# Kernel optimization log

Hardware: AMD Instinct MI355X
Metric: run time of the kernel (lower is better)

## Reference

```python
import jax, jax.numpy as jnp
import numpy as np

PYR = 40000
N_PV, N_OLM, N_BIST = 2100, 1800, 1200
N_SEPT = 100
DT = 1.0
E_EXC, E_INH = 3.0, -0.5


def _sparse_uniform(key, n_out, n_in, conn, w_max, no_autapse=False):
    km, kw = jax.random.split(key)
    mask = jax.random.uniform(km, (n_out, n_in)) < conn
    w = jnp.where(mask, jax.random.uniform(kw, (n_out, n_in)) * w_max, 0.0)
    if no_autapse:
        w = w * (1.0 - jnp.eye(n_out))
    return w.astype(jnp.float32)


def setup_inputs() -> dict:
    key = jax.random.key(0)
    ks = jax.random.split(key, 24)
    inp = {}
    inp['pyr_spikes'] = jax.random.randint(ks[0], (PYR,), 0, 2, dtype=jnp.int32)
    inp['septal_gaba'] = jax.random.uniform(ks[1], (N_SEPT,), dtype=jnp.float32)
    inp['external_exc'] = jax.random.uniform(ks[2], (N_PV,), dtype=jnp.float32)
    inp['prev_pv_spikes'] = (jax.random.uniform(ks[3], (N_PV,)) < 0.1).astype(jnp.float32)
    inp['prev_olm_spikes'] = (jax.random.uniform(ks[4], (N_OLM,)) < 0.1).astype(jnp.float32)
    inp['prev_pv_v_mem'] = jax.random.uniform(ks[5], (N_PV,), dtype=jnp.float32)
    inp['pv_v'] = jax.random.uniform(ks[6], (N_PV,), dtype=jnp.float32)
    inp['olm_v'] = jax.random.uniform(ks[7], (N_OLM,), dtype=jnp.float32)
    inp['bist_v'] = jax.random.uniform(ks[8], (N_BIST,), dtype=jnp.float32)
    inp['pv_adapt'] = jnp.zeros((N_PV,), jnp.float32)
    inp['olm_adapt'] = jnp.zeros((N_OLM,), jnp.float32)
    inp['bist_adapt'] = jnp.zeros((N_BIST,), jnp.float32)
    # weights per WeightInitializer.sparse_uniform calls in __init__ (ca1_inhibitory branch)
    inp['pyr_to_pv'] = _sparse_uniform(ks[9], N_PV, PYR, 0.5, 0.0012)
    inp['pyr_to_olm'] = _sparse_uniform(ks[10], N_OLM, PYR, 0.3, 0.0006)
    inp['pyr_to_bist'] = _sparse_uniform(ks[11], N_BIST, PYR, 0.35, 0.0007)
    inp['pv_to_pyr'] = _sparse_uniform(ks[12], PYR, N_PV, 0.5, 0.003)
    inp['pv_to_pyr_gaba_b'] = _sparse_uniform(ks[13], PYR, N_PV, 0.5, 0.003 * 0.15)
    inp['olm_to_pyr'] = _sparse_uniform(ks[14], PYR, N_OLM, 0.5, 0.001)
    inp['bist_to_pyr'] = _sparse_uniform(ks[15], PYR, N_BIST, 0.55, 0.002)
    inp['pv_to_pv'] = _sparse_uniform(ks[16], N_PV, N_PV, 0.3, 0.0005, no_autapse=True)
    inp['olm_to_pv'] = _sparse_uniform(ks[17], N_PV, N_OLM, 0.2, 0.0004)
    gj = _sparse_uniform(ks[18], N_PV, N_PV, 0.5, 0.0003, no_autapse=True)
    inp['pv_gap'] = (gj + gj.T) * 0.5  # symmetrized gap junctions
    inp['septal_to_olm'] = (jnp.abs(jax.random.normal(ks[19], (N_OLM, N_SEPT))) * 0.5).astype(jnp.float32)
    return inp


def _split_exc(g, nmda_ratio=0.3):
    g = jnp.maximum(g, 0.0)  # conductances are nonnegative
    return g * (1.0 - nmda_ratio), g * nmda_ratio


def _lif_step(v, adapt, g_ampa, g_nmda, g_gaba_a, tau_mem, v_th, v_reset, tau_adapt, adapt_inc):
    # conductance-based LIF: leak toward 0 (v_rest), synaptic currents toward reversals
    i_syn = (g_ampa + g_nmda) * (E_EXC - v) + g_gaba_a * (E_INH - v)
    v_new = v + (DT / tau_mem) * (-v + i_syn)
    spk = (v_new >= (v_th + adapt)).astype(v.dtype)
    v_out = jnp.where(spk > 0, v_reset, v_new)
    adapt_new = adapt * (1.0 - DT / tau_adapt) + adapt_inc * spk
    return spk, v_out, adapt_new


def reference(pyr_spikes, septal_gaba, external_exc, prev_pv_spikes, prev_olm_spikes,
              prev_pv_v_mem, pv_v, olm_v, bist_v, pv_adapt, olm_adapt, bist_adapt,
              pyr_to_pv, pyr_to_olm, pyr_to_bist, pv_to_pyr, pv_to_pyr_gaba_b,
              olm_to_pyr, bist_to_pyr, pv_to_pv, olm_to_pv, pv_gap, septal_to_olm):
    pyr_f = pyr_spikes.astype(jnp.float32)
    pv_exc = pyr_to_pv @ pyr_f
    olm_exc = pyr_to_olm @ pyr_f
    bist_exc = pyr_to_bist @ pyr_f
    pv_exc_from_pyr = pv_exc
    ext_mean = external_exc.mean()
    pv_exc = pv_exc + ext_mean * 0.3
    olm_exc = olm_exc + ext_mean * 0.1
    bist_exc = bist_exc + ext_mean * 0.2
    olm_g_inh = septal_to_olm @ septal_gaba
    pv_lateral = pv_to_pv @ prev_pv_spikes
    olm_to_pv_inhib = olm_to_pv @ prev_olm_spikes
    pv_exc = pv_exc - pv_lateral * 0.5 - olm_to_pv_inhib * 0.3
    # gap junctions: gated by mean pyramidal drive (traced condition -> where)
    drive = pv_exc_from_pyr.mean()
    gain = jnp.where(drive > 0.01, jnp.minimum(1.0, drive / 0.1), 0.0)
    pv_gap_current = pv_gap @ prev_pv_v_mem  # v @ W.T with symmetric-ish W
    pv_exc = pv_exc + pv_gap_current * 0.05 * gain
    pv_ga, pv_gn = _split_exc(pv_exc)
    olm_ga, olm_gn = _split_exc(olm_exc)
    bi_ga, bi_gn = _split_exc(bist_exc)
    zero_pv = jnp.zeros_like(pv_v)
    zero_bi = jnp.zeros_like(bist_v)
    pv_spk, _, _ = _lif_step(pv_v, pv_adapt, pv_ga, pv_gn, zero_pv, 7.0, 2.0, 0.0, 50.0, 0.05)
    olm_spk, _, _ = _lif_step(olm_v, olm_adapt, olm_ga, olm_gn, olm_g_inh, 25.0, 1.1, 0.0, 100.0, 0.2)
    bist_spk, _, _ = _lif_step(bist_v, bist_adapt, bi_ga, bi_gn, zero_bi, 12.0, 0.9, 0.0, 60.0, 0.08)
    perisomatic = pv_to_pyr @ pv_spk
    perisomatic_gaba_b = pv_to_pyr_gaba_b @ pv_spk
    olm_dendritic = olm_to_pyr @ olm_spk
    dendritic = olm_dendritic + bist_to_pyr @ bist_spk
    return (perisomatic, perisomatic_gaba_b, dendritic, olm_dendritic, pv_spk, olm_spk, bist_spk)
```

## Files before the change

### kernel.cpp

```cpp
#include <hip/hip_runtime.h>

#define PYR 40000
#define N_PV 2100
#define N_OLM 1800
#define N_BIST 1200
#define N_SEPT 100

#define WS_PV_RAW   0
#define WS_OLM_RAW  2100
#define WS_BIST_RAW 3900
#define WS_PV_LAT   5100
#define WS_OLM_IPV  7200
#define WS_GAP      9300
#define WS_OLM_GINH 11400

#define O_PERI 0
#define O_GABA 40000
#define O_DEND 80000
#define O_OLMD 120000
#define O_PVS  160000
#define O_OLMS 162100
#define O_BIS  163900

typedef float f4 __attribute__((ext_vector_type(4)));
typedef int   i4 __attribute__((ext_vector_type(4)));

__device__ __forceinline__ f4 ntload(const f4* p) { return __builtin_nontemporal_load(p); }

__device__ __forceinline__ float wave_reduce(float acc) {
    #pragma unroll
    for (int o = 32; o > 0; o >>= 1) acc += __shfl_down(acc, o, 64);
    return acc;
}

#define P1_BLOCKS (N_PV + N_OLM + N_BIST)
#define SMALL_BLOCKS ((3 * N_PV + N_OLM + 3) / 4)
__global__ __launch_bounds__(256) void k_big(
    const float* __restrict__ Wpv, const float* __restrict__ Wolm,
    const float* __restrict__ Wbi, const int* __restrict__ pyr,
    const float* __restrict__ Wpvpv, const float* __restrict__ Wolmpv,
    const float* __restrict__ Wgap,  const float* __restrict__ Wsept,
    const float* __restrict__ prev_pv, const float* __restrict__ prev_olm,
    const float* __restrict__ prev_vm, const float* __restrict__ sept_g,
    float* __restrict__ ws)
{
    int b = blockIdx.x;
    if (b < P1_BLOCKS) {
        const float* W; float* dst;
        if (b < N_PV)               { W = Wpv  + (size_t)b * PYR;                   dst = ws + WS_PV_RAW  + b; }
        else if (b < N_PV + N_OLM)  { int r = b - N_PV;         W = Wolm + (size_t)r * PYR; dst = ws + WS_OLM_RAW  + r; }
        else                        { int r = b - N_PV - N_OLM; W = Wbi  + (size_t)r * PYR; dst = ws + WS_BIST_RAW + r; }

        const f4* W4 = (const f4*)W;
        const i4* S4 = (const i4*)pyr;
        float acc = 0.0f;
        for (int j = threadIdx.x; j < PYR / 4; j += 256) {
            f4 w = ntload(W4 + j);
            i4 s = S4[j];
            acc += w.x * (float)s.x + w.y * (float)s.y + w.z * (float)s.z + w.w * (float)s.w;
        }
        acc = wave_reduce(acc);
        __shared__ float sm[4];
        int lane = threadIdx.x & 63, wv = threadIdx.x >> 6;
        if (lane == 0) sm[wv] = acc;
        __syncthreads();
        if (threadIdx.x == 0) *dst = sm[0] + sm[1] + sm[2] + sm[3];
        return;
    }
    int r = (b - P1_BLOCKS) * 4 + (threadIdx.x >> 6);
    int lane = threadIdx.x & 63;
    const float* W; const float* v; int len4; float* dst;
    if (r < N_PV)                   { W = Wpvpv  + (size_t)r * N_PV;               v = prev_pv;  len4 = N_PV / 4;   dst = ws + WS_PV_LAT  + r; }
    else if (r < 2 * N_PV)          { int i = r - N_PV;     W = Wolmpv + (size_t)i * N_OLM;  v = prev_olm; len4 = N_OLM / 4;  dst = ws + WS_OLM_IPV + i; }
    else if (r < 3 * N_PV)          { int i = r - 2 * N_PV; W = Wgap   + (size_t)i * N_PV;   v = prev_vm;  len4 = N_PV / 4;   dst = ws + WS_GAP     + i; }
    else if (r < 3 * N_PV + N_OLM)  { int i = r - 3 * N_PV; W = Wsept  + (size_t)i * N_SEPT; v = sept_g;   len4 = N_SEPT / 4; dst = ws + WS_OLM_GINH + i; }
    else return;

    const f4* W4 = (const f4*)W;
    const f4* V4 = (const f4*)v;
    float acc = 0.0f;
    for (int j = lane; j < len4; j += 64) {
        f4 w = ntload(W4 + j), x = V4[j];
        acc += w.x * x.x + w.y * x.y + w.z * x.z + w.w * x.w;
    }
    acc = wave_reduce(acc);
    if (lane == 0) *dst = acc;
}

__global__ __launch_bounds__(256) void k_lif(
    const float* __restrict__ ws, const float* __restrict__ ext,
    const float* __restrict__ pv_v,  const float* __restrict__ olm_v,  const float* __restrict__ bist_v,
    const float* __restrict__ pv_ad, const float* __restrict__ olm_ad, const float* __restrict__ bist_ad,
    float* __restrict__ out)
{
    __shared__ float s1[256], s2[256];
    float a = 0.0f, bsum = 0.0f;
    for (int i = threadIdx.x; i < N_PV; i += 256) { a += ext[i]; bsum += ws[WS_PV_RAW + i]; }
    s1[threadIdx.x] = a; s2[threadIdx.x] = bsum;
    __syncthreads();
    for (int o = 128; o > 0; o >>= 1) {
        if (threadIdx.x < o) { s1[threadIdx.x] += s1[threadIdx.x + o]; s2[threadIdx.x] += s2[threadIdx.x + o]; }
        __syncthreads();
    }
    float ext_mean = s1[0] / (float)N_PV;
    float drive    = s2[0] / (float)N_PV;
    float gain = (drive > 0.01f) ? fminf(1.0f, drive / 0.1f) : 0.0f;

    int t = blockIdx.x * 256 + threadIdx.x;
    if (t < N_PV) {
        float g = ws[WS_PV_RAW + t] + ext_mean * 0.3f
                - ws[WS_PV_LAT + t] * 0.5f - ws[WS_OLM_IPV + t] * 0.3f
                + ws[WS_GAP + t] * 0.05f * gain;
        g = fmaxf(g, 0.0f);
        float v = pv_v[t], ad = pv_ad[t];
        float isyn = g * (3.0f - v);
        float vn = v + (1.0f / 7.0f) * (-v + isyn);
        out[O_PVS + t] = (vn >= 2.0f + ad) ? 1.0f : 0.0f;
    } else if (t < N_PV + N_OLM) {
        int i = t - N_PV;
        float g = fmaxf(ws[WS_OLM_RAW + i] + ext_mean * 0.1f, 0.0f);
        float gi = ws[WS_OLM_GINH + i];
        float v = olm_v[i], ad = olm_ad[i];
        float isyn = g * (3.0f - v) + gi * (-0.5f - v);
        float vn = v + (1.0f / 25.0f) * (-v + isyn);
        out[O_OLMS + i] = (vn >= 1.1f + ad) ? 1.0f : 0.0f;
    } else if (t < N_PV + N_OLM + N_BIST) {
        int i = t - N_PV - N_OLM;
        float g = fmaxf(ws[WS_BIST_RAW + i] + ext_mean * 0.2f, 0.0f);
        float v = bist_v[i], ad = bist_ad[i];
        float isyn = g * (3.0f - v);
        float vn = v + (1.0f / 12.0f) * (-v + isyn);
        out[O_BIS + i] = (vn >= 0.9f + ad) ? 1.0f : 0.0f;
    }
}

__global__ __launch_bounds__(256) void k_phase2(
    const float* __restrict__ Wpp, const float* __restrict__ Wppb,
    const float* __restrict__ Wop, const float* __restrict__ Wbp,
    float* __restrict__ out)
{
    int r = blockIdx.x * 4 + (threadIdx.x >> 6);
    int lane = threadIdx.x & 63;
    int job = r / PYR;
    int p = r - job * PYR;

    if (job < 2) {
        const float* W = (job == 0 ? Wpp : Wppb) + (size_t)p * N_PV;
        const f4* W4 = (const f4*)W;
        const f4* V4 = (const f4*)(out + O_PVS);
        float acc = 0.0f;
        for (int j = lane; j < N_PV / 4; j += 64) {
            f4 w = ntload(W4 + j), x = V4[j];
            acc += w.x * x.x + w.y * x.y + w.z * x.z + w.w * x.w;
        }
        acc = wave_reduce(acc);
        if (lane == 0) out[(job == 0 ? O_PERI : O_GABA) + p] = acc;
    } else {
        const f4* Wo4 = (const f4*)(Wop + (size_t)p * N_OLM);
        const f4* Wb4 = (const f4*)(Wbp + (size_t)p * N_BIST);
        const f4* Vo4 = (const f4*)(out + O_OLMS);
        const f4* Vb4 = (const f4*)(out + O_BIS);
        float ao = 0.0f, ab = 0.0f;
        for (int j = lane; j < N_OLM / 4; j += 64) {
            f4 w = ntload(Wo4 + j), x = Vo4[j];
            ao += w.x * x.x + w.y * x.y + w.z * x.z + w.w * x.w;
        }
        for (int j = lane; j < N_BIST / 4; j += 64) {
            f4 w = ntload(Wb4 + j), x = Vb4[j];
            ab += w.x * x.x + w.y * x.y + w.z * x.z + w.w * x.w;
        }
        ao = wave_reduce(ao);
        ab = wave_reduce(ab);
        if (lane == 0) {
            out[O_OLMD + p] = ao;
            out[O_DEND + p] = ao + ab;
        }
    }
}

extern "C" void kernel_launch(void* const* d_in, const int* in_sizes, int n_in,
                              void* d_out, int out_size, void* d_ws, size_t ws_size,
                              hipStream_t stream)
{
    const int*   pyr     = (const int*)  d_in[0];
    const float* sept_g  = (const float*)d_in[1];
    const float* ext     = (const float*)d_in[2];
    const float* prev_pv = (const float*)d_in[3];
    const float* prev_olm= (const float*)d_in[4];
    const float* prev_vm = (const float*)d_in[5];
    const float* pv_v    = (const float*)d_in[6];
    const float* olm_v   = (const float*)d_in[7];
    const float* bist_v  = (const float*)d_in[8];
    const float* pv_ad   = (const float*)d_in[9];
    const float* olm_ad  = (const float*)d_in[10];
    const float* bist_ad = (const float*)d_in[11];
    const float* Wpyr_pv = (const float*)d_in[12];
    const float* Wpyr_olm= (const float*)d_in[13];
    const float* Wpyr_bi = (const float*)d_in[14];
    const float* Wpp     = (const float*)d_in[15];
    const float* Wppb    = (const float*)d_in[16];
    const float* Wop     = (const float*)d_in[17];
    const float* Wbp     = (const float*)d_in[18];
    const float* Wpvpv   = (const float*)d_in[19];
    const float* Wolmpv  = (const float*)d_in[20];
    const float* Wgap    = (const float*)d_in[21];
    const float* Wsept   = (const float*)d_in[22];

    float* ws  = (float*)d_ws;
    float* out = (float*)d_out;

    k_big<<<P1_BLOCKS + SMALL_BLOCKS, 256, 0, stream>>>(
        Wpyr_pv, Wpyr_olm, Wpyr_bi, pyr,
        Wpvpv, Wolmpv, Wgap, Wsept,
        prev_pv, prev_olm, prev_vm, sept_g, ws);
    k_lif<<<(N_PV + N_OLM + N_BIST + 255) / 256, 256, 0, stream>>>(
        ws, ext, pv_v, olm_v, bist_v, pv_ad, olm_ad, bist_ad, out);
    k_phase2<<<(3 * PYR) / 4, 256, 0, stream>>>(Wpp, Wppb, Wop, Wbp, out);
}
```

Measured before the change: 334.2 us.

## Fuse LIF step into first kernel via last-block atomic counter; unroll dot loops

The separate LIF kernel is removed. Its work now runs in the last block of the first kernel to finish, which detects itself with an atomic counter and thread fences, so one launch and its gap go away. Dot-product loops use compile-time trip counts with unrolling, which should give more loads in flight. This adds a memset launch, a serial LIF tail run by a single block, and atomic and fence overhead on every block.

```diff
diff --git a/kernel.cpp b/kernel.cpp
--- a/kernel.cpp
+++ b/kernel.cpp
@@ -13,6 +13,7 @@
 #define WS_OLM_IPV  7200
 #define WS_GAP      9300
 #define WS_OLM_GINH 11400
+#define WS_CNT      13200
 
 #define O_PERI 0
 #define O_GABA 40000
@@ -33,8 +34,31 @@
     return acc;
 }
 
+template<int LEN4>
+__device__ __forceinline__ float dot_row(const f4* __restrict__ W4,
+                                         const f4* __restrict__ V4, int lane) {
+    float acc = 0.0f;
+    constexpr int FULL = LEN4 / 64;
+    constexpr int TAIL = LEN4 % 64;
+    #pragma unroll
+    for (int it = 0; it < FULL; ++it) {
+        int j = lane + it * 64;
+        f4 w = ntload(W4 + j), x = V4[j];
+        acc += w.x * x.x + w.y * x.y + w.z * x.z + w.w * x.w;
+    }
+    if (TAIL && lane < TAIL) {
+        int j = FULL * 64 + lane;
+        f4 w = ntload(W4 + j), x = V4[j];
+        acc += w.x * x.x + w.y * x.y + w.z * x.z + w.w * x.w;
+    }
+    return acc;
+}
+
 #define P1_BLOCKS (N_PV + N_OLM + N_BIST)
-#define SMALL_BLOCKS ((3 * N_PV + N_OLM + 3) / 4)
+#define SMALL_ROWS (3 * N_PV + N_OLM)
+#define SMALL_BLOCKS ((SMALL_ROWS + 3) / 4)
+#define TOTAL_BLOCKS (P1_BLOCKS + SMALL_BLOCKS)
+
 __global__ __launch_bounds__(256) void k_big(
     const float* __restrict__ Wpv, const float* __restrict__ Wolm,
     const float* __restrict__ Wbi, const int* __restrict__ pyr,
@@ -42,9 +66,18 @@
     const float* __restrict__ Wgap,  const float* __restrict__ Wsept,
     const float* __restrict__ prev_pv, const float* __restrict__ prev_olm,
     const float* __restrict__ prev_vm, const float* __restrict__ sept_g,
-    float* __restrict__ ws)
+    const float* __restrict__ ext,
+    const float* __restrict__ pv_v,  const float* __restrict__ olm_v,  const float* __restrict__ bist_v,
+    const float* __restrict__ pv_ad, const float* __restrict__ olm_ad, const float* __restrict__ bist_ad,
+    float* __restrict__ ws, float* __restrict__ out, int* __restrict__ counter)
 {
+    __shared__ float sm[4];
+    __shared__ int   is_last;
+    __shared__ float s1[256], s2[256];
+
     int b = blockIdx.x;
+    int lane = threadIdx.x & 63;
+
     if (b < P1_BLOCKS) {
         const float* W; float* dst;
         if (b < N_PV)               { W = Wpv  + (size_t)b * PYR;                   dst = ws + WS_PV_RAW  + b; }
@@ -54,49 +87,59 @@
         const f4* W4 = (const f4*)W;
         const i4* S4 = (const i4*)pyr;
         float acc = 0.0f;
-        for (int j = threadIdx.x; j < PYR / 4; j += 256) {
+        #pragma unroll 4
+        for (int it = 0; it < 39; ++it) {
+            int j = threadIdx.x + it * 256;
             f4 w = ntload(W4 + j);
             i4 s = S4[j];
             acc += w.x * (float)s.x + w.y * (float)s.y + w.z * (float)s.z + w.w * (float)s.w;
         }
+        if (threadIdx.x < 16) {
+            int j = 9984 + threadIdx.x;
+            f4 w = ntload(W4 + j);
+            i4 s = S4[j];
+            acc += w.x * (float)s.x + w.y * (float)s.y + w.z * (float)s.z + w.w * (float)s.w;
+        }
         acc = wave_reduce(acc);
-        __shared__ float sm[4];
-        int lane = threadIdx.x & 63, wv = threadIdx.x >> 6;
+        int wv = threadIdx.x >> 6;
         if (lane == 0) sm[wv] = acc;
         __syncthreads();
         if (threadIdx.x == 0) *dst = sm[0] + sm[1] + sm[2] + sm[3];
-        return;
-    }
-    int r = (b - P1_BLOCKS) * 4 + (threadIdx.x >> 6);
-    int lane = threadIdx.x & 63;
-    const float* W; const float* v; int len4; float* dst;
-    if (r < N_PV)                   { W = Wpvpv  + (size_t)r * N_PV;               v = prev_pv;  len4 = N_PV / 4;   dst = ws + WS_PV_LAT  + r; }
-    else if (r < 2 * N_PV)          { int i = r - N_PV;     W = Wolmpv + (size_t)i * N_OLM;  v = prev_olm; len4 = N_OLM / 4;  dst = ws + WS_OLM_IPV + i; }
-    else if (r < 3 * N_PV)          { int i = r - 2 * N_PV; W = Wgap   + (size_t)i * N_PV;   v = prev_vm;  len4 = N_PV / 4;   dst = ws + WS_GAP     + i; }
-    else if (r < 3 * N_PV + N_OLM)  { int i = r - 3 * N_PV; W = Wsept  + (size_t)i * N_SEPT; v = sept_g;   len4 = N_SEPT / 4; dst = ws + WS_OLM_GINH + i; }
-    else return;
-
-    const f4* W4 = (const f4*)W;
-    const f4* V4 = (const f4*)v;
-    float acc = 0.0f;
-    for (int j = lane; j < len4; j += 64) {
-        f4 w = ntload(W4 + j), x = V4[j];
-        acc += w.x * x.x + w.y * x.y + w.z * x.z + w.w * x.w;
-    }
-    acc = wave_reduce(acc);
-    if (lane == 0) *dst = acc;
-}
-
-__global__ __launch_bounds__(256) void k_lif(
-    const float* __restrict__ ws, const float* __restrict__ ext,
-    const float* __restrict__ pv_v,  const float* __restrict__ olm_v,  const float* __restrict__ bist_v,
-    const float* __restrict__ pv_ad, const float* __restrict__ olm_ad, const float* __restrict__ bist_ad,
-    float* __restrict__ out)
-{
-    __shared__ float s1[256], s2[256];
-    float a = 0.0f, bsum = 0.0f;
-    for (int i = threadIdx.x; i < N_PV; i += 256) { a += ext[i]; bsum += ws[WS_PV_RAW + i]; }
-    s1[threadIdx.x] = a; s2[threadIdx.x] = bsum;
+    } else {
+        int r = (b - P1_BLOCKS) * 4 + (threadIdx.x >> 6);
+        float res = 0.0f; float* dst = nullptr;
+        if (r < N_PV) {
+            dst = ws + WS_PV_LAT + r;
+            res = dot_row<525>((const f4*)(Wpvpv + (size_t)r * N_PV), (const f4*)prev_pv, lane);
+        } else if (r < 2 * N_PV) {
+            int i = r - N_PV; dst = ws + WS_OLM_IPV + i;
+            res = dot_row<450>((const f4*)(Wolmpv + (size_t)i * N_OLM), (const f4*)prev_olm, lane);
+        } else if (r < 3 * N_PV) {
+            int i = r - 2 * N_PV; dst = ws + WS_GAP + i;
+            res = dot_row<525>((const f4*)(Wgap + (size_t)i * N_PV), (const f4*)prev_vm, lane);
+        } else if (r < SMALL_ROWS) {
+            int i = r - 3 * N_PV; dst = ws + WS_OLM_GINH + i;
+            res = dot_row<25>((const f4*)(Wsept + (size_t)i * N_SEPT), (const f4*)sept_g, lane);
+        }
+        if (dst) {
+            res = wave_reduce(res);
+            if (lane == 0) *dst = res;
+        }
+    }
+
+    __syncthreads();
+    if (threadIdx.x == 0) {
+        __threadfence();
+        int old = atomicAdd(counter, 1);
+        is_last = (old == TOTAL_BLOCKS - 1) ? 1 : 0;
+    }
+    __syncthreads();
+    if (!is_last) return;
+    __threadfence();
+
+    float a = 0.0f, bs = 0.0f;
+    for (int i = threadIdx.x; i < N_PV; i += 256) { a += ext[i]; bs += ws[WS_PV_RAW + i]; }
+    s1[threadIdx.x] = a; s2[threadIdx.x] = bs;
     __syncthreads();
     for (int o = 128; o > 0; o >>= 1) {
         if (threadIdx.x < o) { s1[threadIdx.x] += s1[threadIdx.x + o]; s2[threadIdx.x] += s2[threadIdx.x + o]; }
@@ -106,31 +149,29 @@
     float drive    = s2[0] / (float)N_PV;
     float gain = (drive > 0.01f) ? fminf(1.0f, drive / 0.1f) : 0.0f;
 
-    int t = blockIdx.x * 256 + threadIdx.x;
-    if (t < N_PV) {
-        float g = ws[WS_PV_RAW + t] + ext_mean * 0.3f
-                - ws[WS_PV_LAT + t] * 0.5f - ws[WS_OLM_IPV + t] * 0.3f
-                + ws[WS_GAP + t] * 0.05f * gain;
-        g = fmaxf(g, 0.0f);
-        float v = pv_v[t], ad = pv_ad[t];
-        float isyn = g * (3.0f - v);
-        float vn = v + (1.0f / 7.0f) * (-v + isyn);
-        out[O_PVS + t] = (vn >= 2.0f + ad) ? 1.0f : 0.0f;
-    } else if (t < N_PV + N_OLM) {
-        int i = t - N_PV;
-        float g = fmaxf(ws[WS_OLM_RAW + i] + ext_mean * 0.1f, 0.0f);
-        float gi = ws[WS_OLM_GINH + i];
-        float v = olm_v[i], ad = olm_ad[i];
-        float isyn = g * (3.0f - v) + gi * (-0.5f - v);
-        float vn = v + (1.0f / 25.0f) * (-v + isyn);
-        out[O_OLMS + i] = (vn >= 1.1f + ad) ? 1.0f : 0.0f;
-    } else if (t < N_PV + N_OLM + N_BIST) {
-        int i = t - N_PV - N_OLM;
-        float g = fmaxf(ws[WS_BIST_RAW + i] + ext_mean * 0.2f, 0.0f);
-        float v = bist_v[i], ad = bist_ad[i];
-        float isyn = g * (3.0f - v);
-        float vn = v + (1.0f / 12.0f) * (-v + isyn);
-        out[O_BIS + i] = (vn >= 0.9f + ad) ? 1.0f : 0.0f;
+    for (int t = threadIdx.x; t < N_PV + N_OLM + N_BIST; t += 256) {
+        if (t < N_PV) {
+            float g = ws[WS_PV_RAW + t] + ext_mean * 0.3f
+                    - ws[WS_PV_LAT + t] * 0.5f - ws[WS_OLM_IPV + t] * 0.3f
+                    + ws[WS_GAP + t] * 0.05f * gain;
+            g = fmaxf(g, 0.0f);
+            float v = pv_v[t], ad = pv_ad[t];
+            float vn = v + (1.0f / 7.0f) * (-v + g * (3.0f - v));
+            out[O_PVS + t] = (vn >= 2.0f + ad) ? 1.0f : 0.0f;
+        } else if (t < N_PV + N_OLM) {
+            int i = t - N_PV;
+            float g = fmaxf(ws[WS_OLM_RAW + i] + ext_mean * 0.1f, 0.0f);
+            float gi = ws[WS_OLM_GINH + i];
+            float v = olm_v[i], ad = olm_ad[i];
+            float vn = v + (1.0f / 25.0f) * (-v + g * (3.0f - v) + gi * (-0.5f - v));
+            out[O_OLMS + i] = (vn >= 1.1f + ad) ? 1.0f : 0.0f;
+        } else {
+            int i = t - N_PV - N_OLM;
+            float g = fmaxf(ws[WS_BIST_RAW + i] + ext_mean * 0.2f, 0.0f);
+            float v = bist_v[i], ad = bist_ad[i];
+            float vn = v + (1.0f / 12.0f) * (-v + g * (3.0f - v));
+            out[O_BIS + i] = (vn >= 0.9f + ad) ? 1.0f : 0.0f;
+        }
     }
 }
 
@@ -146,29 +187,12 @@
 
     if (job < 2) {
         const float* W = (job == 0 ? Wpp : Wppb) + (size_t)p * N_PV;
-        const f4* W4 = (const f4*)W;
-        const f4* V4 = (const f4*)(out + O_PVS);
-        float acc = 0.0f;
-        for (int j = lane; j < N_PV / 4; j += 64) {
-            f4 w = ntload(W4 + j), x = V4[j];
-            acc += w.x * x.x + w.y * x.y + w.z * x.z + w.w * x.w;
-        }
+        float acc = dot_row<525>((const f4*)W, (const f4*)(out + O_PVS), lane);
         acc = wave_reduce(acc);
         if (lane == 0) out[(job == 0 ? O_PERI : O_GABA) + p] = acc;
     } else {
-        const f4* Wo4 = (const f4*)(Wop + (size_t)p * N_OLM);
-        const f4* Wb4 = (const f4*)(Wbp + (size_t)p * N_BIST);
-        const f4* Vo4 = (const f4*)(out + O_OLMS);
-        const f4* Vb4 = (const f4*)(out + O_BIS);
-        float ao = 0.0f, ab = 0.0f;
-        for (int j = lane; j < N_OLM / 4; j += 64) {
-            f4 w = ntload(Wo4 + j), x = Vo4[j];
-            ao += w.x * x.x + w.y * x.y + w.z * x.z + w.w * x.w;
-        }
-        for (int j = lane; j < N_BIST / 4; j += 64) {
-            f4 w = ntload(Wb4 + j), x = Vb4[j];
-            ab += w.x * x.x + w.y * x.y + w.z * x.z + w.w * x.w;
-        }
+        float ao = dot_row<450>((const f4*)(Wop + (size_t)p * N_OLM),  (const f4*)(out + O_OLMS), lane);
+        float ab = dot_row<300>((const f4*)(Wbp + (size_t)p * N_BIST), (const f4*)(out + O_BIS),  lane);
         ao = wave_reduce(ao);
         ab = wave_reduce(ab);
         if (lane == 0) {
@@ -208,12 +232,15 @@
 
     float* ws  = (float*)d_ws;
     float* out = (float*)d_out;
-
-    k_big<<<P1_BLOCKS + SMALL_BLOCKS, 256, 0, stream>>>(
+    int* counter = (int*)(ws + WS_CNT);
+
+    hipMemsetAsync(counter, 0, sizeof(int), stream);
+
+    k_big<<<TOTAL_BLOCKS, 256, 0, stream>>>(
         Wpyr_pv, Wpyr_olm, Wpyr_bi, pyr,
         Wpvpv, Wolmpv, Wgap, Wsept,
-        prev_pv, prev_olm, prev_vm, sept_g, ws);
-    k_lif<<<(N_PV + N_OLM + N_BIST + 255) / 256, 256, 0, stream>>>(
-        ws, ext, pv_v, olm_v, bist_v, pv_ad, olm_ad, bist_ad, out);
+        prev_pv, prev_olm, prev_vm, sept_g,
+        ext, pv_v, olm_v, bist_v, pv_ad, olm_ad, bist_ad,
+        ws, out, counter);
     k_phase2<<<(3 * PYR) / 4, 256, 0, stream>>>(Wpp, Wppb, Wop, Wbp, out);
 }
```

Result: slower. 687.4 us (+105.7%).
